# Optimization experiments

Measured on AMD Instinct MI355X. Metric: run time of the kernel, lower is better.

Reference implementation:

```python
import jax, jax.numpy as jnp
import numpy as np

B, L = 16384, 50
NUM_LABELS, EMBED_DIM = 100000, 32

def setup_inputs() -> dict:
    key = jax.random.key(0)
    k1, k2, k3 = jax.random.split(key, 3)
    embed_table = jax.random.normal(k1, (NUM_LABELS, EMBED_DIM), dtype=jnp.float32)
    indices = jax.random.randint(k2, (B, L), 0, NUM_LABELS, dtype=jnp.int64)
    # lengths in [0, L]; length-0 bags produce zero embeddings (as in the torch code)
    lengths = jax.random.randint(k3, (B,), 0, L + 1, dtype=jnp.int64)
    return {"embed_table": embed_table, "indices": indices, "lengths": lengths}

def reference(embed_table, indices, lengths):
    # mask[b, l] = l < lengths[b]  -> valid slots of each ragged bag
    mask = (jnp.arange(L)[None, :] < lengths[:, None])  # [B, L] bool
    gathered = embed_table[indices]                      # [B, L, D] gather
    summed = jnp.sum(gathered * mask[:, :, None].astype(embed_table.dtype), axis=1)  # [B, D]
    denom = jnp.maximum(lengths, 1).astype(embed_table.dtype)[:, None]
    # empty bags: sum is 0, so result is exactly zeros (matches torch.zeros branch)
    return summed / denom
```

## Files before the change

### kernel.cpp

```cpp
#include <hip/hip_runtime.h>


#define BAGS      16384
#define BAG_LEN   50
#define EMB_DIM   32

__global__ __launch_bounds__(256) void multilabel_embed_kernel(
    const float* __restrict__ table,
    const int*   __restrict__ indices,
    const int*   __restrict__ lengths,
    float*       __restrict__ out)
{
    const int wavesPerBlock = blockDim.x >> 6;
    int bag = blockIdx.x * wavesPerBlock + (threadIdx.x >> 6);
    bag = __builtin_amdgcn_readfirstlane(bag);
    if (bag >= BAGS) return;

    const int lane = threadIdx.x & 63;
    const int sub  = (lane & 7) << 2;
    const int eg   = lane >> 3;

    int len = lengths[bag];
    len = __builtin_amdgcn_readfirstlane(len);
    if (len < 0) len = 0;
    if (len > BAG_LEN) len = BAG_LEN;

    const int* __restrict__ idx = indices + bag * BAG_LEN;

    float4 acc = make_float4(0.f, 0.f, 0.f, 0.f);
    for (int base = 0; base < len; base += 16) {
        const int l0 = base + eg;
        const int l1 = base + 8 + eg;
        const int i0 = idx[(l0 < len) ? l0 : 0];
        const int i1 = idx[(l1 < len) ? l1 : 0];
        const float4 r0 = *reinterpret_cast<const float4*>(
            table + (size_t)i0 * EMB_DIM + sub);
        const float4 r1 = *reinterpret_cast<const float4*>(
            table + (size_t)i1 * EMB_DIM + sub);
        const bool v0 = (l0 < len), v1 = (l1 < len);
        acc.x += v0 ? r0.x : 0.f;  acc.y += v0 ? r0.y : 0.f;
        acc.z += v0 ? r0.z : 0.f;  acc.w += v0 ? r0.w : 0.f;
        acc.x += v1 ? r1.x : 0.f;  acc.y += v1 ? r1.y : 0.f;
        acc.z += v1 ? r1.z : 0.f;  acc.w += v1 ? r1.w : 0.f;
    }

#pragma unroll
    for (int m = 8; m < 64; m <<= 1) {
        acc.x += __shfl_xor(acc.x, m);
        acc.y += __shfl_xor(acc.y, m);
        acc.z += __shfl_xor(acc.z, m);
        acc.w += __shfl_xor(acc.w, m);
    }

    if (eg == 0) {
        const float inv = 1.0f / (float)(len > 0 ? len : 1);
        acc.x *= inv; acc.y *= inv; acc.z *= inv; acc.w *= inv;
        *reinterpret_cast<float4*>(out + (size_t)bag * EMB_DIM + sub) = acc;
    }
}

extern "C" void kernel_launch(void* const* d_in, const int* in_sizes, int n_in,
                              void* d_out, int out_size, void* d_ws, size_t ws_size,
                              hipStream_t stream) {
    const float* table   = (const float*)d_in[0];
    const int*   indices = (const int*)d_in[1];
    const int*   lengths = (const int*)d_in[2];
    float*       out     = (float*)d_out;

    const int threads = 256;
    const int grid = BAGS / 4;

    multilabel_embed_kernel<<<grid, threads, 0, stream>>>(table, indices, lengths, out);
}
```

Before: 14.67 us.

## Load bag indices once per wave and fully unroll gathers with shuffles

Each lane now loads one index of the bag in a single coalesced read, and per-step indices are handed out with wave shuffles instead of dependent scalar loads inside the loop. The loop over the bag is fully unrolled to seven steps, so all row gathers are issued before any accumulation, which exposes more memory-level parallelism. In exchange, short bags still issue all seven gathers (invalid slots fetch row idx[0] and are masked out), which adds redundant memory traffic, and register use goes up.

```diff
diff --git a/kernel.cpp b/kernel.cpp
--- a/kernel.cpp
+++ b/kernel.cpp
@@ -4,6 +4,7 @@
 #define BAGS      16384
 #define BAG_LEN   50
 #define EMB_DIM   32
+#define NSTEP     7
 
 __global__ __launch_bounds__(256) void multilabel_embed_kernel(
     const float* __restrict__ table,
@@ -26,22 +27,32 @@
     if (len > BAG_LEN) len = BAG_LEN;
 
     const int* __restrict__ idx = indices + bag * BAG_LEN;
+    const int myidx = idx[(lane < BAG_LEN) ? lane : (BAG_LEN - 1)];
+
+    int  ix[NSTEP];
+    bool valid[NSTEP];
+#pragma unroll
+    for (int s = 0; s < NSTEP; ++s) {
+        const int l = s * 8 + eg;
+        valid[s] = (l < len);
+        const int cl = valid[s] ? l : 0;
+        ix[s] = __shfl(myidx, cl);
+    }
+
+    float4 r[NSTEP];
+#pragma unroll
+    for (int s = 0; s < NSTEP; ++s) {
+        r[s] = *reinterpret_cast<const float4*>(
+            table + (size_t)ix[s] * EMB_DIM + sub);
+    }
 
     float4 acc = make_float4(0.f, 0.f, 0.f, 0.f);
-    for (int base = 0; base < len; base += 16) {
-        const int l0 = base + eg;
-        const int l1 = base + 8 + eg;
-        const int i0 = idx[(l0 < len) ? l0 : 0];
-        const int i1 = idx[(l1 < len) ? l1 : 0];
-        const float4 r0 = *reinterpret_cast<const float4*>(
-            table + (size_t)i0 * EMB_DIM + sub);
-        const float4 r1 = *reinterpret_cast<const float4*>(
-            table + (size_t)i1 * EMB_DIM + sub);
-        const bool v0 = (l0 < len), v1 = (l1 < len);
-        acc.x += v0 ? r0.x : 0.f;  acc.y += v0 ? r0.y : 0.f;
-        acc.z += v0 ? r0.z : 0.f;  acc.w += v0 ? r0.w : 0.f;
-        acc.x += v1 ? r1.x : 0.f;  acc.y += v1 ? r1.y : 0.f;
-        acc.z += v1 ? r1.z : 0.f;  acc.w += v1 ? r1.w : 0.f;
+#pragma unroll
+    for (int s = 0; s < NSTEP; ++s) {
+        acc.x += valid[s] ? r[s].x : 0.f;
+        acc.y += valid[s] ? r[s].y : 0.f;
+        acc.z += valid[s] ? r[s].z : 0.f;
+        acc.w += valid[s] ? r[s].w : 0.f;
     }
 
 #pragma unroll
```

Result: faster. 13.48 us (median of 2 runs) (-8.1%).
